# Performance work log

Hardware: AMD Instinct MI355X
Metric: run time of the kernel (lower is better)

## Reference

```python
import jax, jax.numpy as jnp
import numpy as np

B, LAT, D = 64, 256, 64           # batch, latent dim, voxel grid side (== output image side)
ALPHA_ADJ = float(np.log2(D) + 2)  # alpha_adjust = log2(output_img_shape[0]) + 2


def _rotmat(a):
    """3x3 rotation matrix from Euler angles (x,y,z), R = Rz @ Ry @ Rx."""
    cx, sx = jnp.cos(a[0]), jnp.sin(a[0])
    cy, sy = jnp.cos(a[1]), jnp.sin(a[1])
    cz, sz = jnp.cos(a[2]), jnp.sin(a[2])
    Rx = jnp.array([[1, 0, 0], [0, 0, 0], [0, 0, 0]], jnp.float32).at[1, 1].set(cx).at[1, 2].set(-sx).at[2, 1].set(sx).at[2, 2].set(cx)
    Ry = jnp.array([[0, 0, 0], [0, 1, 0], [0, 0, 0]], jnp.float32).at[0, 0].set(cy).at[0, 2].set(sy).at[2, 0].set(-sy).at[2, 2].set(cy)
    Rz = jnp.array([[0, 0, 0], [0, 0, 0], [0, 0, 1]], jnp.float32).at[0, 0].set(cz).at[0, 1].set(-sz).at[1, 0].set(sz).at[1, 1].set(cz)
    return Rz @ Ry @ Rx


def _apply_transform(vol, R):
    """Rotate a [D,D,D] volume about its centre via trilinear sampling, zero padding."""
    d = vol.shape[0]
    c = (d - 1) / 2.0
    idx = jnp.arange(d, dtype=jnp.float32)
    gi, gj, gk = jnp.meshgrid(idx, idx, idx, indexing='ij')
    dst = jnp.stack([gi, gj, gk], axis=-1) - c        # [D,D,D,3]
    src = dst @ R.T + c                                # source coords
    x, y, z = src[..., 0], src[..., 1], src[..., 2]
    x0 = jnp.floor(x); y0 = jnp.floor(y); z0 = jnp.floor(z)
    fx, fy, fz = x - x0, y - y0, z - z0

    def gather(ix, iy, iz):
        valid = (ix >= 0) & (ix < d) & (iy >= 0) & (iy < d) & (iz >= 0) & (iz < d)
        ixc = jnp.clip(ix, 0, d - 1).astype(jnp.int32)
        iyc = jnp.clip(iy, 0, d - 1).astype(jnp.int32)
        izc = jnp.clip(iz, 0, d - 1).astype(jnp.int32)
        return jnp.where(valid, vol[ixc, iyc, izc], 0.0)

    c000 = gather(x0, y0, z0);     c001 = gather(x0, y0, z0 + 1)
    c010 = gather(x0, y0 + 1, z0); c011 = gather(x0, y0 + 1, z0 + 1)
    c100 = gather(x0 + 1, y0, z0); c101 = gather(x0 + 1, y0, z0 + 1)
    c110 = gather(x0 + 1, y0 + 1, z0); c111 = gather(x0 + 1, y0 + 1, z0 + 1)
    c00 = c000 * (1 - fz) + c001 * fz
    c01 = c010 * (1 - fz) + c011 * fz
    c10 = c100 * (1 - fz) + c101 * fz
    c11 = c110 * (1 - fz) + c111 * fz
    c0 = c00 * (1 - fy) + c01 * fy
    c1 = c10 * (1 - fy) + c11 * fy
    return c0 * (1 - fx) + c1 * fx


def setup_inputs() -> dict:
    key = jax.random.key(0)
    k1, k2, k3 = jax.random.split(key, 3)
    encoded = jax.random.normal(k1, (B, LAT), dtype=jnp.float32)
    W = jax.random.normal(k2, (LAT, D * D * D), dtype=jnp.float32) * 0.02
    b = jnp.zeros((D * D * D,), jnp.float32)
    angles = jax.random.uniform(k3, (B, 3), jnp.float32, -np.pi, np.pi)
    return {"encoded": encoded, "W": W, "b": b, "angles": angles}


def reference(encoded, W, b, angles):
    # voxel_generator: linear -> sigmoid -> [B, D, D, D], then alpha sharpening
    voxels = jax.nn.sigmoid(encoded @ W + b).reshape(B, D, D, D)
    voxels = voxels ** ALPHA_ADJ
    R = jax.vmap(_rotmat)(angles)                       # [B,3,3]
    views = jax.vmap(_apply_transform)(voxels, R)       # [B,D,D,D]
    # alpha compositing back-to-front along last (depth) axis
    alphas = jnp.moveaxis(views, -1, 0)[:, :, None]     # [Dz, B, 1, H, W]
    def step(img, a):
        return img * (1 - a) + a, None
    images, _ = jax.lax.scan(step, jnp.zeros((B, 1, D, D), jnp.float32), alphas, reverse=True)
    return 2 * images - 1
```

## Files before the change

### kernel.cpp

```cpp
#include <hip/hip_runtime.h>
#include <hip/hip_bf16.h>
#include <hip/hip_fp16.h>
#include <math.h>

#define BATCH 64
#define LAT   256
#define DVOX  64
#define VOX   (DVOX*DVOX*DVOX)

typedef __attribute__((ext_vector_type(8))) short short8;
typedef __attribute__((ext_vector_type(4))) float f32x4;
typedef unsigned uint32x4 __attribute__((ext_vector_type(4), aligned(4)));

__global__ void prep_kernel(const float* __restrict__ enc,
                            const float* __restrict__ angles,
                            unsigned short* __restrict__ encB,
                            float* __restrict__ Rmat) {
    int tid = threadIdx.x;
    for (int idx = tid; idx < BATCH * LAT; idx += blockDim.x) {
        __hip_bfloat16 h = __float2bfloat16(enc[idx]);
        encB[idx] = *reinterpret_cast<unsigned short*>(&h);
    }
    if (tid < BATCH) {
        float ax = angles[tid*3+0], ay = angles[tid*3+1], az = angles[tid*3+2];
        float cx = cosf(ax), sx = sinf(ax);
        float cy = cosf(ay), sy = sinf(ay);
        float cz = cosf(az), sz = sinf(az);
        float* R = Rmat + tid * 9;
        R[0] = cz*cy;  R[1] = cz*sy*sx - sz*cx;  R[2] = cz*sy*cx + sz*sx;
        R[3] = sz*cy;  R[4] = sz*sy*sx + cz*cx;  R[5] = sz*sy*cx - cz*sx;
        R[6] = -sy;    R[7] = cy*sx;             R[8] = cy*cx;
    }
}

#define KT    32
#define LROW  260
#define LBUF  8352

__device__ __forceinline__ void gload_lds16(const float* g, unsigned* l) {
    __builtin_amdgcn_global_load_lds(
        (__attribute__((address_space(1))) void*)(g),
        (__attribute__((address_space(3))) void*)(l),
        16, 0, 0);
}

__global__ __launch_bounds__(256, 2) void gemm_mfma_kernel(
        const unsigned short* __restrict__ encB,
        const float* __restrict__ W,
        const float* __restrict__ bias,
        __half* __restrict__ vox) {
    __shared__ unsigned lds[2 * LBUF];

    int wave = threadIdx.x >> 6;
    int lane = threadIdx.x & 63;
    int l15 = lane & 15, l4 = lane >> 4;
    int n0 = blockIdx.x * 256;
    int n4 = n0 + wave * 64 + 4 * l15;

    const unsigned short* ap = encB + l15 * LAT + l4 * 8;
    const float* gb = W + n0 + lane * 4;

    f32x4 acc[4][4];
#pragma unroll
    for (int t = 0; t < 4; ++t)
#pragma unroll
        for (int mt = 0; mt < 4; ++mt) acc[t][mt] = (f32x4){0.f, 0.f, 0.f, 0.f};

    auto stage = [&](int buf, int kb) {
        unsigned* lb = lds + buf * LBUF;
#pragma unroll
        for (int i = 0; i < 8; ++i) {
            int row = i * 4 + wave;
            gload_lds16(gb + (size_t)(kb + row) * VOX,
                        lb + row * LROW + ((row >> 3) & 3) * 8);
        }
    };

    stage(0, 0);

#pragma unroll
    for (int kt = 0; kt < 8; ++kt) {
        __syncthreads();
        if (kt < 7) stage((kt + 1) & 1, (kt + 1) * KT);

        short8 a[4];
#pragma unroll
        for (int mt = 0; mt < 4; ++mt)
            a[mt] = *(const short8*)(ap + mt * 16 * LAT + kt * KT);

        const unsigned* lb = lds + (kt & 1) * LBUF
                           + (l4 * 8) * LROW + l4 * 8
                           + wave * 64 + 4 * l15;
        uint4 dj[8];
#pragma unroll
        for (int j = 0; j < 8; ++j)
            dj[j] = *(const uint4*)(lb + j * LROW);

        short8 bf[4];
#pragma unroll
        for (int t = 0; t < 4; ++t) {
            unsigned bw[4];
#pragma unroll
            for (int dw = 0; dw < 4; ++dw) {
                unsigned u0 = ((const unsigned*)&dj[2 * dw])[t]     + 0x8000u;
                unsigned u1 = ((const unsigned*)&dj[2 * dw + 1])[t] + 0x8000u;
                bw[dw] = __builtin_amdgcn_perm(u1, u0, 0x07060302u);
            }
            bf[t] = *reinterpret_cast<short8*>(bw);
        }
#pragma unroll
        for (int t = 0; t < 4; ++t)
#pragma unroll
            for (int mt = 0; mt < 4; ++mt)
                acc[t][mt] = __builtin_amdgcn_mfma_f32_16x16x32_bf16(a[mt], bf[t], acc[t][mt], 0, 0, 0);
    }

    float4 bv = *(const float4*)(bias + n4);
#pragma unroll
    for (int mt = 0; mt < 4; ++mt) {
#pragma unroll
        for (int r = 0; r < 4; ++r) {
            int b = mt * 16 + l4 * 4 + r;
            float s[4];
#pragma unroll
            for (int t = 0; t < 4; ++t) {
                float x = acc[t][mt][r] + ((const float*)&bv)[t];
                float v = 1.f / (1.f + __expf(-x));
                v = v * v; v = v * v; v = v * v;
                s[t] = v;
            }
            __half2 h01 = __floats2half2_rn(s[0], s[1]);
            __half2 h23 = __floats2half2_rn(s[2], s[3]);
            uint2 pk;
            pk.x = *reinterpret_cast<unsigned*>(&h01);
            pk.y = *reinterpret_cast<unsigned*>(&h23);
            *reinterpret_cast<uint2*>(vox + (size_t)b * VOX + n4) = pk;
        }
    }
}

__device__ __forceinline__ float zlerp(unsigned e, float fz) {
    __half2 h = *reinterpret_cast<__half2*>(&e);
    float2 f = __half22float2(h);
    return f.x + (f.y - f.x) * fz;
}

__global__ __launch_bounds__(256) void render_lds_kernel(
        const __half* __restrict__ vox,
        const float* __restrict__ Rmat,
        float* __restrict__ out) {
    __shared__ unsigned sV[16 * 16 * 17];
    __shared__ float sT[4][64], sE[4][64];

    int bid  = blockIdx.x;
    int b    = bid & 63;
    int tile = bid >> 6;
    int t    = threadIdx.x;
    int pix  = t & 63, seg = t >> 6;
    int i0 = (tile >> 3) * 8, j0 = (tile & 7) * 8;
    int i = i0 + (pix >> 3);
    int j = j0 + (pix & 7);

    const float* Rb = Rmat + b * 9;
    float R0 = Rb[0], R1 = Rb[1], R2 = Rb[2];
    float R3 = Rb[3], R4 = Rb[4], R5 = Rb[5];
    float R6 = Rb[6], R7 = Rb[7], R8 = Rb[8];

    const float c = (DVOX - 1) * 0.5f;
    float di = (float)i - c, dj = (float)j - c;
    float xb = fmaf(R0, di, fmaf(R1, dj, c));
    float yb = fmaf(R3, di, fmaf(R4, dj, c));
    float zb = fmaf(R6, di, fmaf(R7, dj, c));

    float dic = (float)i0 + 3.5f - c;
    float djc = (float)j0 + 3.5f - c;
    float hwx = 3.5f * (fabsf(R0) + fabsf(R1) + fabsf(R2)) + 1e-3f;
    float hwy = 3.5f * (fabsf(R3) + fabsf(R4) + fabsf(R5)) + 1e-3f;
    float hwz = 3.5f * (fabsf(R6) + fabsf(R7) + fabsf(R8)) + 1e-3f;

    const unsigned short* V = (const unsigned short*)vox + (size_t)b * VOX;

    int rx = t >> 4, ry = t & 15;
    unsigned d[9];
    int xlo_n, ylo_n, zlo_n, s_n;

    auto bbox = [&](int ch) {
        float dkc = (float)(ch * 8) + 3.5f - c;
        float xc = fmaf(R0, dic, fmaf(R1, djc, fmaf(R2, dkc, c)));
        float yc = fmaf(R3, dic, fmaf(R4, djc, fmaf(R5, dkc, c)));
        float zc = fmaf(R6, dic, fmaf(R7, djc, fmaf(R8, dkc, c)));
        xlo_n = (int)floorf(xc - hwx);
        ylo_n = (int)floorf(yc - hwy);
        zlo_n = (int)floorf(zc - hwz);
        s_n   = zlo_n & ~1;
    };
    auto issue = [&]() {
        int gxc = min(max(xlo_n + rx, 0), DVOX - 1);
        int gyc = min(max(ylo_n + ry, 0), DVOX - 1);
        const unsigned* p = (const unsigned*)(V + ((gxc << 12) + (gyc << 6) + s_n));
        uint32x4 q0 = *(const uint32x4*)p;
        uint32x4 q1 = *(const uint32x4*)(p + 4);
        unsigned q2 = p[8];
        d[0] = q0[0]; d[1] = q0[1]; d[2] = q0[2]; d[3] = q0[3];
        d[4] = q1[0]; d[5] = q1[1]; d[6] = q1[2]; d[7] = q1[3];
        d[8] = q2;
    };

    bbox(7); issue();
    int xlo = xlo_n, ylo = ylo_n, zlo = zlo_n, s = s_n;

    float img = 0.f;
#pragma unroll 1
    for (int ch = 7; ch >= 0; --ch) {
        bool zint = (zlo >= 0) && (zlo + 17 <= DVOX);

        {
            bool rv = ((unsigned)(xlo + rx) < (unsigned)DVOX) &
                      ((unsigned)(ylo + ry) < (unsigned)DVOX);
            unsigned tt[9];
#pragma unroll
            for (int k = 0; k < 9; ++k) tt[k] = d[k];
            if (!zint) {
#pragma unroll
                for (int k = 0; k < 9; ++k) {
                    int h0 = s + 2 * k;
                    unsigned m = (((unsigned)h0 < (unsigned)DVOX) ? 0x0000FFFFu : 0u)
                               | (((unsigned)(h0 + 1) < (unsigned)DVOX) ? 0xFFFF0000u : 0u);
                    tt[k] &= m;
                }
            }
            unsigned rvm = rv ? 0xFFFFFFFFu : 0u;
#pragma unroll
            for (int k = 0; k < 9; ++k) tt[k] &= rvm;

            unsigned A[8];
#pragma unroll
            for (int m = 0; m < 8; ++m)
                A[m] = (tt[m] >> 16) | (tt[m + 1] << 16);

            unsigned* wrow = sV + t * 17;
            if (zlo & 1) {
#pragma unroll
                for (int m = 0; m < 8; ++m) {
                    wrow[2 * m]     = A[m];
                    wrow[2 * m + 1] = tt[m + 1];
                }
            } else {
#pragma unroll
                for (int m = 0; m < 8; ++m) {
                    wrow[2 * m]     = tt[m];
                    wrow[2 * m + 1] = A[m];
                }
            }
        }
        __syncthreads();

        if (ch > 0) { bbox(ch - 1); issue(); }

        float T = 1.f, E = 0.f;
        int k0 = ch * 8;
#pragma unroll
        for (int q = 1; q >= 0; --q) {
            int kk = 2 * seg + q;
            float dk = (float)(k0 + kk) - c;
            float x = fmaf(R2, dk, xb);
            float y = fmaf(R5, dk, yb);
            float z = fmaf(R8, dk, zb);

            float xf = floorf(x), yf = floorf(y), zf = floorf(z);
            float fx = x - xf, fy = y - yf, fz = z - zf;
            int xi = (int)xf - xlo;
            int yi = (int)yf - ylo;
            int zi = (int)zf - zlo;
            const unsigned* e = sV + (xi * 272 + yi * 17 + zi);

            float c00 = zlerp(e[0],   fz);
            float c01 = zlerp(e[17],  fz);
            float c10 = zlerp(e[272], fz);
            float c11 = zlerp(e[289], fz);
            float c0 = c00 + (c01 - c00) * fy;
            float c1 = c10 + (c11 - c10) * fy;
            float a  = c0  + (c1  - c0 ) * fx;

            E = E * (1.f - a) + a;
            T *= (1.f - a);
        }
        sT[seg][pix] = T;
        sE[seg][pix] = E;
        __syncthreads();

        if (seg == 0) {
            float im = img;
#pragma unroll
            for (int ss = 3; ss >= 0; --ss)
                im = fmaf(sT[ss][pix], im, sE[ss][pix]);
            img = im;
        }

        xlo = xlo_n; ylo = ylo_n; zlo = zlo_n; s = s_n;
    }

    if (seg == 0)
        out[b * (DVOX * DVOX) + i * DVOX + j] = 2.f * img - 1.f;
}

extern "C" void kernel_launch(void* const* d_in, const int* in_sizes, int n_in,
                              void* d_out, int out_size, void* d_ws, size_t ws_size,
                              hipStream_t stream) {
    const float* enc    = (const float*)d_in[0];
    const float* W      = (const float*)d_in[1];
    const float* bias   = (const float*)d_in[2];
    const float* angles = (const float*)d_in[3];
    float* out = (float*)d_out;

    char* ws = (char*)d_ws;
    unsigned short* encB = (unsigned short*)ws;
    float* Rmat          = (float*)(ws + 32768);
    __half* vox          = (__half*)(ws + 65536);

    prep_kernel<<<1, 256, 0, stream>>>(enc, angles, encB, Rmat);
    gemm_mfma_kernel<<<VOX / 256, 256, 0, stream>>>(encB, W, bias, vox);
    render_lds_kernel<<<BATCH * 64, 256, 0, stream>>>(vox, Rmat, out);
}
```

Measured before the change: 142.2 us.

## Widen GEMM tile to 1024 columns with 8 waves, single-buffered LDS

Restructures the voxel GEMM so each block covers 1024 output columns with 512 threads, and each wave handles 128 columns (8 MFMA N-tiles per wave instead of 4). Double buffering is removed: every K-step stages a tile, syncs, computes, then syncs again. This cuts the block count and raises per-wave MFMA work per LDS read, and the epilogue writes 16-byte stores. In exchange, the global load of W is no longer overlapped with compute, and the larger accumulator set raises register pressure at 512 threads per block.

```diff
diff --git a/kernel.cpp b/kernel.cpp
--- a/kernel.cpp
+++ b/kernel.cpp
@@ -11,6 +11,7 @@
 typedef __attribute__((ext_vector_type(8))) short short8;
 typedef __attribute__((ext_vector_type(4))) float f32x4;
 typedef unsigned uint32x4 __attribute__((ext_vector_type(4), aligned(4)));
+typedef unsigned u32x4 __attribute__((ext_vector_type(4)));
 
 __global__ void prep_kernel(const float* __restrict__ enc,
                             const float* __restrict__ angles,
@@ -33,9 +34,7 @@
     }
 }
 
-#define KT    32
-#define LROW  260
-#define LBUF  8352
+#define RS 1032
 
 __device__ __forceinline__ void gload_lds16(const float* g, unsigned* l) {
     __builtin_amdgcn_global_load_lds(
@@ -44,97 +43,96 @@
         16, 0, 0);
 }
 
-__global__ __launch_bounds__(256, 2) void gemm_mfma_kernel(
+__global__ __launch_bounds__(512, 2) void gemm_mfma_kernel(
         const unsigned short* __restrict__ encB,
         const float* __restrict__ W,
         const float* __restrict__ bias,
         __half* __restrict__ vox) {
-    __shared__ unsigned lds[2 * LBUF];
+    extern __shared__ unsigned lds[];
 
     int wave = threadIdx.x >> 6;
     int lane = threadIdx.x & 63;
     int l15 = lane & 15, l4 = lane >> 4;
-    int n0 = blockIdx.x * 256;
-    int n4 = n0 + wave * 64 + 4 * l15;
-
-    const unsigned short* ap = encB + l15 * LAT + l4 * 8;
-    const float* gb = W + n0 + lane * 4;
-
-    f32x4 acc[4][4];
-#pragma unroll
-    for (int t = 0; t < 4; ++t)
+    int n0 = blockIdx.x * 1024;
+    int cd = wave * 128 + l15 * 8;
+
+    f32x4 acc[8][4];
+#pragma unroll
+    for (int t = 0; t < 8; ++t)
 #pragma unroll
         for (int mt = 0; mt < 4; ++mt) acc[t][mt] = (f32x4){0.f, 0.f, 0.f, 0.f};
 
-    auto stage = [&](int buf, int kb) {
-        unsigned* lb = lds + buf * LBUF;
-#pragma unroll
-        for (int i = 0; i < 8; ++i) {
-            int row = i * 4 + wave;
-            gload_lds16(gb + (size_t)(kb + row) * VOX,
-                        lb + row * LROW + ((row >> 3) & 3) * 8);
+    auto stage = [&](int kt) {
+#pragma unroll
+        for (int wi = 0; wi < 16; ++wi) {
+            int idx = wave * 16 + wi;
+            int r   = idx >> 2;
+            int ch  = idx & 3;
+            gload_lds16(W + (size_t)(kt * 32 + r) * VOX + n0 + ch * 256 + lane * 4,
+                        lds + r * RS + ch * 256);
         }
     };
 
-    stage(0, 0);
-
-#pragma unroll
+#pragma unroll 1
     for (int kt = 0; kt < 8; ++kt) {
+        stage(kt);
         __syncthreads();
-        if (kt < 7) stage((kt + 1) & 1, (kt + 1) * KT);
 
         short8 a[4];
 #pragma unroll
         for (int mt = 0; mt < 4; ++mt)
-            a[mt] = *(const short8*)(ap + mt * 16 * LAT + kt * KT);
-
-        const unsigned* lb = lds + (kt & 1) * LBUF
-                           + (l4 * 8) * LROW + l4 * 8
-                           + wave * 64 + 4 * l15;
-        uint4 dj[8];
-#pragma unroll
-        for (int j = 0; j < 8; ++j)
-            dj[j] = *(const uint4*)(lb + j * LROW);
-
-        short8 bf[4];
-#pragma unroll
-        for (int t = 0; t < 4; ++t) {
-            unsigned bw[4];
-#pragma unroll
-            for (int dw = 0; dw < 4; ++dw) {
-                unsigned u0 = ((const unsigned*)&dj[2 * dw])[t]     + 0x8000u;
-                unsigned u1 = ((const unsigned*)&dj[2 * dw + 1])[t] + 0x8000u;
-                bw[dw] = __builtin_amdgcn_perm(u1, u0, 0x07060302u);
+            a[mt] = *(const short8*)(encB + (mt * 16 + l15) * LAT + kt * 32 + l4 * 8);
+
+        unsigned bfw[8][4];
+#pragma unroll
+        for (int jp = 0; jp < 4; ++jp) {
+            const unsigned* base = lds + (l4 * 8 + 2 * jp) * RS + cd;
+            u32x4 q0 = *(const u32x4*)(base);
+            u32x4 q1 = *(const u32x4*)(base + 4);
+            u32x4 q2 = *(const u32x4*)(base + RS);
+            u32x4 q3 = *(const u32x4*)(base + RS + 4);
+#pragma unroll
+            for (int t4 = 0; t4 < 4; ++t4) {
+                bfw[t4][jp]     = __builtin_amdgcn_perm(q2[t4] + 0x8000u, q0[t4] + 0x8000u, 0x07060302u);
+                bfw[t4 + 4][jp] = __builtin_amdgcn_perm(q3[t4] + 0x8000u, q1[t4] + 0x8000u, 0x07060302u);
             }
-            bf[t] = *reinterpret_cast<short8*>(bw);
-        }
-#pragma unroll
-        for (int t = 0; t < 4; ++t)
+        }
+#pragma unroll
+        for (int t = 0; t < 8; ++t) {
+            short8 bf = *reinterpret_cast<short8*>(bfw[t]);
 #pragma unroll
             for (int mt = 0; mt < 4; ++mt)
-                acc[t][mt] = __builtin_amdgcn_mfma_f32_16x16x32_bf16(a[mt], bf[t], acc[t][mt], 0, 0, 0);
-    }
-
-    float4 bv = *(const float4*)(bias + n4);
+                acc[t][mt] = __builtin_amdgcn_mfma_f32_16x16x32_bf16(a[mt], bf, acc[t][mt], 0, 0, 0);
+        }
+        __syncthreads();
+    }
+
+    float4 bv0 = *(const float4*)(bias + n0 + cd);
+    float4 bv1 = *(const float4*)(bias + n0 + cd + 4);
 #pragma unroll
     for (int mt = 0; mt < 4; ++mt) {
 #pragma unroll
         for (int r = 0; r < 4; ++r) {
             int b = mt * 16 + l4 * 4 + r;
-            float s[4];
-#pragma unroll
-            for (int t = 0; t < 4; ++t) {
-                float x = acc[t][mt][r] + ((const float*)&bv)[t];
+            float s[8];
+#pragma unroll
+            for (int t = 0; t < 8; ++t) {
+                float bvt = (t < 4) ? ((const float*)&bv0)[t] : ((const float*)&bv1)[t - 4];
+                float x = acc[t][mt][r] + bvt;
                 float v = 1.f / (1.f + __expf(-x));
                 v = v * v; v = v * v; v = v * v;
                 s[t] = v;
             }
-            __half2 h01 = __floats2half2_rn(s[0], s[1]);
-            __half2 h23 = __floats2half2_rn(s[2], s[3]);
-            uint2 pk;
-            pk.x = *reinterpret_cast<unsigned*>(&h01);
-            pk.y = *reinterpret_cast<unsigned*>(&h23);
-            *reinterpret_cast<uint2*>(vox + (size_t)b * VOX + n4) = pk;
+            __half2 h0 = __floats2half2_rn(s[0], s[1]);
+            __half2 h1 = __floats2half2_rn(s[2], s[3]);
+            __half2 h2 = __floats2half2_rn(s[4], s[5]);
+            __half2 h3 = __floats2half2_rn(s[6], s[7]);
+            uint32x4 pk;
+            pk[0] = *reinterpret_cast<unsigned*>(&h0);
+            pk[1] = *reinterpret_cast<unsigned*>(&h1);
+            pk[2] = *reinterpret_cast<unsigned*>(&h2);
+            pk[3] = *reinterpret_cast<unsigned*>(&h3);
+            *reinterpret_cast<uint32x4*>(vox + (size_t)b * VOX + n0 + cd) = pk;
         }
     }
 }
@@ -319,6 +317,6 @@
     __half* vox          = (__half*)(ws + 65536);
 
     prep_kernel<<<1, 256, 0, stream>>>(enc, angles, encB, Rmat);
-    gemm_mfma_kernel<<<VOX / 256, 256, 0, stream>>>(encB, W, bias, vox);
+    gemm_mfma_kernel<<<VOX / 1024, 512, 32 * RS * 4, stream>>>(encB, W, bias, vox);
     render_lds_kernel<<<BATCH * 64, 256, 0, stream>>>(vox, Rmat, out);
 }
```

New measurement: 143.5 us. No clear change (+0.9%).

## Triple-buffer GEMM W staging with explicit vmcnt waits and prefetch depth two

Applied to the files above, without the earlier changes.

The GEMM main loop now keeps three LDS buffers and prefetches both the A fragments and the W tiles two k-steps ahead. It uses hand-placed s_waitcnt vmcnt counts and raw s_barrier calls in place of __syncthreads. The goal is to hide more of the global W streaming latency behind MFMA work. In exchange, LDS use per block rises to about 100KB of dynamic shared memory and the launch-bounds occupancy hint is dropped, which may lower occupancy. The hard-coded wait counts assume a particular order and number of memory instructions emitted by the compiler.

```diff
diff --git a/kernel.cpp b/kernel.cpp
--- a/kernel.cpp
+++ b/kernel.cpp
@@ -33,9 +33,8 @@
     }
 }
 
-#define KT    32
-#define LROW  260
-#define LBUF  8352
+#define LROW 260
+#define LBUF 8352
 
 __device__ __forceinline__ void gload_lds16(const float* g, unsigned* l) {
     __builtin_amdgcn_global_load_lds(
@@ -44,12 +43,12 @@
         16, 0, 0);
 }
 
-__global__ __launch_bounds__(256, 2) void gemm_mfma_kernel(
+__global__ __launch_bounds__(256) void gemm_mfma_kernel(
         const unsigned short* __restrict__ encB,
         const float* __restrict__ W,
         const float* __restrict__ bias,
         __half* __restrict__ vox) {
-    __shared__ unsigned lds[2 * LBUF];
+    extern __shared__ unsigned lds[];
 
     int wave = threadIdx.x >> 6;
     int lane = threadIdx.x & 63;
@@ -66,7 +65,14 @@
 #pragma unroll
         for (int mt = 0; mt < 4; ++mt) acc[t][mt] = (f32x4){0.f, 0.f, 0.f, 0.f};
 
-    auto stage = [&](int buf, int kb) {
+    short8 a[3][4];
+
+    auto loadA = [&](short8* as, int kb) {
+#pragma unroll
+        for (int mt = 0; mt < 4; ++mt)
+            as[mt] = *(const short8*)(ap + mt * 16 * LAT + kb);
+    };
+    auto stageW = [&](int buf, int kb) {
         unsigned* lb = lds + buf * LBUF;
 #pragma unroll
         for (int i = 0; i < 8; ++i) {
@@ -75,27 +81,14 @@
                         lb + row * LROW + ((row >> 3) & 3) * 8);
         }
     };
-
-    stage(0, 0);
-
-#pragma unroll
-    for (int kt = 0; kt < 8; ++kt) {
-        __syncthreads();
-        if (kt < 7) stage((kt + 1) & 1, (kt + 1) * KT);
-
-        short8 a[4];
-#pragma unroll
-        for (int mt = 0; mt < 4; ++mt)
-            a[mt] = *(const short8*)(ap + mt * 16 * LAT + kt * KT);
-
-        const unsigned* lb = lds + (kt & 1) * LBUF
+    auto compute = [&](int buf, const short8* as) {
+        const unsigned* lb = lds + buf * LBUF
                            + (l4 * 8) * LROW + l4 * 8
                            + wave * 64 + 4 * l15;
         uint4 dj[8];
 #pragma unroll
         for (int j = 0; j < 8; ++j)
             dj[j] = *(const uint4*)(lb + j * LROW);
-
         short8 bf[4];
 #pragma unroll
         for (int t = 0; t < 4; ++t) {
@@ -112,8 +105,35 @@
         for (int t = 0; t < 4; ++t)
 #pragma unroll
             for (int mt = 0; mt < 4; ++mt)
-                acc[t][mt] = __builtin_amdgcn_mfma_f32_16x16x32_bf16(a[mt], bf[t], acc[t][mt], 0, 0, 0);
-    }
+                acc[t][mt] = __builtin_amdgcn_mfma_f32_16x16x32_bf16(as[mt], bf[t], acc[t][mt], 0, 0, 0);
+    };
+
+    loadA(a[0], 0);   stageW(0, 0);
+    loadA(a[1], 32);  stageW(1, 32);
+
+#define KSTEP(kt, WAITSTR)                                        \
+    {                                                             \
+        if ((kt) + 2 < 8) {                                       \
+            loadA(a[((kt) + 2) % 3], ((kt) + 2) * 32);            \
+            stageW(((kt) + 2) % 3, ((kt) + 2) * 32);              \
+        }                                                         \
+        asm volatile(WAITSTR ::: "memory");                       \
+        __builtin_amdgcn_sched_barrier(0);                        \
+        __builtin_amdgcn_s_barrier();                             \
+        __builtin_amdgcn_sched_barrier(0);                        \
+        compute((kt) % 3, a[(kt) % 3]);                           \
+        __builtin_amdgcn_s_barrier();                             \
+    }
+
+    KSTEP(0, "s_waitcnt vmcnt(24)")
+    KSTEP(1, "s_waitcnt vmcnt(24)")
+    KSTEP(2, "s_waitcnt vmcnt(24)")
+    KSTEP(3, "s_waitcnt vmcnt(24)")
+    KSTEP(4, "s_waitcnt vmcnt(24)")
+    KSTEP(5, "s_waitcnt vmcnt(24)")
+    KSTEP(6, "s_waitcnt vmcnt(12)")
+    KSTEP(7, "s_waitcnt vmcnt(0)")
+#undef KSTEP
 
     float4 bv = *(const float4*)(bias + n4);
 #pragma unroll
@@ -319,6 +339,6 @@
     __half* vox          = (__half*)(ws + 65536);
 
     prep_kernel<<<1, 256, 0, stream>>>(enc, angles, encB, Rmat);
-    gemm_mfma_kernel<<<VOX / 256, 256, 0, stream>>>(encB, W, bias, vox);
+    gemm_mfma_kernel<<<VOX / 256, 256, 3 * LBUF * 4, stream>>>(encB, W, bias, vox);
     render_lds_kernel<<<BATCH * 64, 256, 0, stream>>>(vox, Rmat, out);
 }
```

After: 154.4 us. +8.6%, slower.
